# Performance work log

Measured on AMD Instinct MI355X. Metric: run time of the kernel, lower is better.

Reference implementation:

```python
import jax, jax.numpy as jnp
import numpy as np

L, H, D, V, TMAX = 12, 12, 768, 50257, 1024
B, T = 2, 1024
HD = D // H
EPS = 1e-5


def new_gelu(x):
    return 0.5 * x * (1.0 + jnp.tanh(jnp.sqrt(2.0 / jnp.pi) * (x + 0.044715 * x ** 3)))


def layer_norm(x, w, b):
    mu = jnp.mean(x, axis=-1, keepdims=True)
    var = jnp.var(x, axis=-1, keepdims=True)
    return (x - mu) * jax.lax.rsqrt(var + EPS) * w + b


def setup_inputs() -> dict:
    key = jax.random.key(0)
    ks = jax.random.split(key, 12)
    s = 0.02
    return {
        "idx": jax.random.randint(ks[0], (B, T), 0, V),
        "wte": jax.random.normal(ks[1], (V, D), jnp.float32) * s,
        "wpe": jax.random.normal(ks[2], (TMAX, D), jnp.float32) * s,
        "ln1_w": jnp.ones((L, D), jnp.float32),
        "ln1_b": jnp.zeros((L, D), jnp.float32),
        "attn_w": jax.random.normal(ks[3], (L, D, 3 * D), jnp.float32) * s,
        "attn_b": jnp.zeros((L, 3 * D), jnp.float32),
        "proj_w": jax.random.normal(ks[4], (L, D, D), jnp.float32) * (s / jnp.sqrt(2.0 * L)),
        "proj_b": jnp.zeros((L, D), jnp.float32),
        "ln2_w": jnp.ones((L, D), jnp.float32),
        "ln2_b": jnp.zeros((L, D), jnp.float32),
        "fc_w": jax.random.normal(ks[5], (L, D, 4 * D), jnp.float32) * s,
        "fc_b": jnp.zeros((L, 4 * D), jnp.float32),
        "fc2_w": jax.random.normal(ks[6], (L, 4 * D, D), jnp.float32) * (s / jnp.sqrt(2.0 * L)),
        "fc2_b": jnp.zeros((L, D), jnp.float32),
        "lnf_w": jnp.ones((D,), jnp.float32),
        "lnf_b": jnp.zeros((D,), jnp.float32),
        "lm_head_w": jax.random.normal(ks[7], (D, V), jnp.float32) * s,
    }


def _gpt_forward(idx, wte, wpe, ln1_w, ln1_b, attn_w, attn_b, proj_w, proj_b,
                 ln2_w, ln2_b, fc_w, fc_b, fc2_w, fc2_b, lnf_w, lnf_b, lm_head_w):
    b, t = idx.shape
    x = wte[idx] + wpe[:t][None, :, :]  # [B,T,D]
    causal = jnp.tril(jnp.ones((t, t), bool))  # [T,T]
    scale = 1.0 / jnp.sqrt(jnp.asarray(HD, x.dtype))

    layer_params = {
        "ln1_w": ln1_w, "ln1_b": ln1_b, "attn_w": attn_w, "attn_b": attn_b,
        "proj_w": proj_w, "proj_b": proj_b, "ln2_w": ln2_w, "ln2_b": ln2_b,
        "fc_w": fc_w, "fc_b": fc_b, "fc2_w": fc2_w, "fc2_b": fc2_b,
    }

    def block(x, p):
        h = layer_norm(x, p["ln1_w"], p["ln1_b"])
        qkv = h @ p["attn_w"] + p["attn_b"]  # [B,T,3D]
        q, k, v = jnp.split(qkv, 3, axis=-1)
        q = q.reshape(b, t, H, HD)
        k = k.reshape(b, t, H, HD)
        v = v.reshape(b, t, H, HD)
        att = jnp.einsum("bqhd,bkhd->bhqk", q, k) * scale
        att = jnp.where(causal[None, None, :, :], att, -jnp.inf)
        att = jax.nn.softmax(att, axis=-1)
        y = jnp.einsum("bhqk,bkhd->bqhd", att, v).reshape(b, t, D)
        x = x + y @ p["proj_w"] + p["proj_b"]
        h2 = layer_norm(x, p["ln2_w"], p["ln2_b"])
        m = new_gelu(h2 @ p["fc_w"] + p["fc_b"])
        x = x + m @ p["fc2_w"] + p["fc2_b"]
        return x, None

    x, _ = jax.lax.scan(block, x, layer_params)
    x = layer_norm(x, lnf_w, lnf_b)
    logits = x @ lm_head_w  # [B,T,V]
    return logits


def reference(idx, wte, wpe, ln1_w, ln1_b, attn_w, attn_b, proj_w, proj_b,
              ln2_w, ln2_b, fc_w, fc_b, fc2_w, fc2_b, lnf_w, lnf_b, lm_head_w):
    return _gpt_forward(idx, wte, wpe, ln1_w, ln1_b, attn_w, attn_b, proj_w, proj_b,
                        ln2_w, ln2_b, fc_w, fc_b, fc2_w, fc2_b, lnf_w, lnf_b, lm_head_w)
```

## Files before the change

kernel.cpp:

```cpp
#include <hip/hip_runtime.h>
#include <math.h>

#define Bsz  2
#define Tlen 1024
#define Dm   768
#define Hh   12
#define HDm  64
#define Ll   12
#define Vv   50257
#define Mrows (Bsz * Tlen)

typedef __attribute__((ext_vector_type(8))) short short8;
typedef __attribute__((ext_vector_type(4))) float f32x4;

__device__ __forceinline__ float bf2f(unsigned short u) {
  union { unsigned int i; float f; } v; v.i = ((unsigned int)u) << 16; return v.f;
}
__device__ __forceinline__ unsigned short f2bf(float f) {
  union { float f; unsigned int i; } v; v.f = f;
  unsigned int u = v.i;
  return (unsigned short)((u + 0x7FFFu + ((u >> 16) & 1u)) >> 16);
}
__device__ __forceinline__ float gelu_f(float x) {
  const float c = 0.7978845608028654f;
  return 0.5f * x * (1.0f + tanhf(c * (x + 0.044715f * x * x * x)));
}

__device__ __forceinline__ void gl_lds16(const unsigned short* g, unsigned short* l) {
  __builtin_amdgcn_global_load_lds(
      (const __attribute__((address_space(1))) unsigned int*)g,
      (__attribute__((address_space(3))) unsigned int*)l, 16, 0, 0);
}

__global__ void embed_kernel(const int* __restrict__ idx, const float* __restrict__ wte,
                             const float* __restrict__ wpe, float* __restrict__ x) {
  int i = (blockIdx.x * 256 + threadIdx.x) * 4;
  int d = i % Dm;
  int bt = i / Dm;
  int t = bt % Tlen;
  int tok = idx[bt];
  float4 a = *(const float4*)(wte + (size_t)tok * Dm + d);
  float4 p = *(const float4*)(wpe + (size_t)t * Dm + d);
  float4 r; r.x = a.x + p.x; r.y = a.y + p.y; r.z = a.z + p.z; r.w = a.w + p.w;
  *(float4*)(x + i) = r;
}

__global__ __launch_bounds__(256) void ln_wave(const float* __restrict__ x,
                                               const float* __restrict__ w,
                                               const float* __restrict__ b,
                                               unsigned short* __restrict__ out) {
  int tid = threadIdx.x, wv = tid >> 6, l = tid & 63;
  int row = blockIdx.x * 4 + wv;
  const float* xr = x + (size_t)row * Dm;
  float4 v[3];
  float s = 0.f, s2 = 0.f;
#pragma unroll
  for (int i = 0; i < 3; ++i) {
    v[i] = *(const float4*)(xr + l * 4 + i * 256);
    s += v[i].x + v[i].y + v[i].z + v[i].w;
    s2 += v[i].x * v[i].x + v[i].y * v[i].y + v[i].z * v[i].z + v[i].w * v[i].w;
  }
#pragma unroll
  for (int o = 1; o < 64; o <<= 1) {
    s += __shfl_xor(s, o, 64);
    s2 += __shfl_xor(s2, o, 64);
  }
  float mu = s * (1.0f / Dm);
  float var = s2 * (1.0f / Dm) - mu * mu;
  float rstd = rsqrtf(var + 1e-5f);
  unsigned short* yr = out + (size_t)row * Dm;
#pragma unroll
  for (int i = 0; i < 3; ++i) {
    float4 wv4 = *(const float4*)(w + l * 4 + i * 256);
    float4 bv4 = *(const float4*)(b + l * 4 + i * 256);
    ushort4 o4;
    o4.x = f2bf((v[i].x - mu) * rstd * wv4.x + bv4.x);
    o4.y = f2bf((v[i].y - mu) * rstd * wv4.y + bv4.y);
    o4.z = f2bf((v[i].z - mu) * rstd * wv4.z + bv4.z);
    o4.w = f2bf((v[i].w - mu) * rstd * wv4.w + bv4.w);
    *(ushort4*)(yr + l * 4 + i * 256) = o4;
  }
}

__global__ __launch_bounds__(256) void tconv_kernel(const float* __restrict__ W, int ldw,
                                                    int nValid, unsigned short* __restrict__ WT,
                                                    int K) {
  __shared__ float S[32][33];
  int n0 = blockIdx.x * 32, k0 = blockIdx.y * 32;
  int t = threadIdx.x;
  int nc = t & 31, kr0 = t >> 5;
#pragma unroll
  for (int i = 0; i < 4; ++i) {
    int kr = kr0 + i * 8;
    S[kr][nc] = (n0 + nc < nValid) ? W[(size_t)(k0 + kr) * ldw + n0 + nc] : 0.f;
  }
  __syncthreads();
  int r = t >> 3, c4 = (t & 7) * 4;
  ushort4 o;
  o.x = f2bf(S[c4 + 0][r]); o.y = f2bf(S[c4 + 1][r]);
  o.z = f2bf(S[c4 + 2][r]); o.w = f2bf(S[c4 + 3][r]);
  *(ushort4*)(WT + (size_t)(n0 + r) * K + k0 + c4) = o;
}

__global__ __launch_bounds__(256) void tconv4_kernel(
    const float* __restrict__ wA, const float* __restrict__ wP,
    const float* __restrict__ wF, const float* __restrict__ wF2,
    unsigned short* __restrict__ oA, unsigned short* __restrict__ oP,
    unsigned short* __restrict__ oF, unsigned short* __restrict__ oF2) {
  int bid = blockIdx.x;
  const float* W; unsigned short* WT; int ldw, K, ntn, local;
  if (bid < 1728)      { W = wA;  WT = oA;  ldw = 2304; K = 768;  ntn = 72; local = bid; }
  else if (bid < 2304) { W = wP;  WT = oP;  ldw = 768;  K = 768;  ntn = 24; local = bid - 1728; }
  else if (bid < 4608) { W = wF;  WT = oF;  ldw = 3072; K = 768;  ntn = 96; local = bid - 2304; }
  else                 { W = wF2; WT = oF2; ldw = 768;  K = 3072; ntn = 24; local = bid - 4608; }
  int n0 = (local % ntn) * 32, k0 = (local / ntn) * 32;
  __shared__ float S[32][33];
  int t = threadIdx.x;
  int nc = t & 31, kr0 = t >> 5;
#pragma unroll
  for (int i = 0; i < 4; ++i) {
    int kr = kr0 + i * 8;
    S[kr][nc] = W[(size_t)(k0 + kr) * ldw + n0 + nc];
  }
  __syncthreads();
  int r = t >> 3, c4 = (t & 7) * 4;
  ushort4 o;
  o.x = f2bf(S[c4 + 0][r]); o.y = f2bf(S[c4 + 1][r]);
  o.z = f2bf(S[c4 + 2][r]); o.w = f2bf(S[c4 + 3][r]);
  *(ushort4*)(WT + (size_t)(n0 + r) * K + k0 + c4) = o;
}

template<bool XMAP>
__global__ __launch_bounds__(256) void gemm_big(
    const unsigned short* __restrict__ A, const unsigned short* __restrict__ B, int K,
    const float* __restrict__ bias, const float* __restrict__ res,
    float* __restrict__ outF, unsigned short* __restrict__ outB,
    int ldc, int nValid, int act, int nColTiles) {
  int brow, bcol;
  if (XMAP) {
    int b = blockIdx.x, xcd = b & 7, slot = b >> 3;
    bcol = xcd + 8 * (slot >> 4);
    brow = slot & 15;
    if (bcol >= nColTiles) return;
  } else {
    bcol = blockIdx.x; brow = blockIdx.y;
  }
  __shared__ alignas(16) unsigned short As[2][128][32];
  __shared__ alignas(16) unsigned short Bs[2][128][32];
  int tid = threadIdx.x;
  int rowBase = brow * 128, colBase = bcol * 128;
  int w = tid >> 6, l = tid & 63;
  int wr = w >> 1, wc = w & 1;
  int srow = tid >> 2, skk = (tid & 3) * 8;
  const unsigned short* aSrc = A + (size_t)(rowBase + srow) * K + skk;
  const unsigned short* bSrc = B + (size_t)(colBase + srow) * K + skk;

  f32x4 acc[4][4];
#pragma unroll
  for (int m = 0; m < 4; ++m)
#pragma unroll
    for (int n = 0; n < 4; ++n) acc[m][n] = (f32x4){0.f, 0.f, 0.f, 0.f};

  int fr = l & 15, fq = l >> 4;

  gl_lds16(aSrc, &As[0][w * 16][0]);
  gl_lds16(aSrc + (size_t)64 * K, &As[0][w * 16 + 64][0]);
  gl_lds16(bSrc, &Bs[0][w * 16][0]);
  gl_lds16(bSrc + (size_t)64 * K, &Bs[0][w * 16 + 64][0]);

  int nIt = K >> 5;
  for (int it = 0; it < nIt; ++it) {
    int cur = it & 1;
    int k0 = it * 32;
    if (it + 1 < nIt) {
      int nx = cur ^ 1;
      gl_lds16(aSrc + k0 + 32, &As[nx][w * 16][0]);
      gl_lds16(aSrc + (size_t)64 * K + k0 + 32, &As[nx][w * 16 + 64][0]);
      gl_lds16(bSrc + k0 + 32, &Bs[nx][w * 16][0]);
      gl_lds16(bSrc + (size_t)64 * K + k0 + 32, &Bs[nx][w * 16 + 64][0]);
      asm volatile("s_waitcnt vmcnt(4)" ::: "memory");
    } else {
      asm volatile("s_waitcnt vmcnt(0)" ::: "memory");
    }
    asm volatile("s_barrier" ::: "memory");

    short8 af[4], bfr[4];
#pragma unroll
    for (int m = 0; m < 4; ++m)
      af[m] = *(const short8*)&As[cur][wr * 64 + m * 16 + fr][fq * 8];
#pragma unroll
    for (int n = 0; n < 4; ++n)
      bfr[n] = *(const short8*)&Bs[cur][wc * 64 + n * 16 + fr][fq * 8];
#pragma unroll
    for (int m = 0; m < 4; ++m)
#pragma unroll
      for (int n = 0; n < 4; ++n)
        acc[m][n] = __builtin_amdgcn_mfma_f32_16x16x32_bf16(af[m], bfr[n], acc[m][n], 0, 0, 0);
    asm volatile("s_barrier" ::: "memory");
  }

#pragma unroll
  for (int m = 0; m < 4; ++m) {
    int row = rowBase + wr * 64 + m * 16 + fq * 4;
#pragma unroll
    for (int n = 0; n < 4; ++n) {
      int col = colBase + wc * 64 + n * 16 + fr;
      if (col >= nValid) continue;
      float bv = bias ? bias[col] : 0.f;
#pragma unroll
      for (int j = 0; j < 4; ++j) {
        float v = acc[m][n][j] + bv;
        if (act) v = gelu_f(v);
        if (res) v += res[(size_t)(row + j) * ldc + col];
        if (outF) outF[(size_t)(row + j) * ldc + col] = v;
        else      outB[(size_t)(row + j) * ldc + col] = f2bf(v);
      }
    }
  }
}

__global__ __launch_bounds__(256) void gemm_bf16_sm(
    const unsigned short* __restrict__ A, const unsigned short* __restrict__ B, int K,
    const float* __restrict__ bias, const float* __restrict__ res,
    float* __restrict__ outF, unsigned short* __restrict__ outB,
    int ldc, int act) {
  __shared__ alignas(16) unsigned short As[2][64][32];
  __shared__ alignas(16) unsigned short Bs[2][128][32];
  int tid = threadIdx.x;
  int rowBase = blockIdx.y * 64;
  int colBase = blockIdx.x * 128;
  int w = tid >> 6, l = tid & 63;
  int fr = l & 15, fq = l >> 4;

  int srow = l >> 2, skk = (l & 3) * 8;
  const unsigned short* aSrc = A + (size_t)(rowBase + w * 16 + srow) * K + skk;
  const unsigned short* bSrc = B + (size_t)(colBase + w * 16 + srow) * K + skk;

  f32x4 acc[4][2];
#pragma unroll
  for (int m = 0; m < 4; ++m)
#pragma unroll
    for (int n = 0; n < 2; ++n) acc[m][n] = (f32x4){0.f, 0.f, 0.f, 0.f};

  gl_lds16(aSrc, &As[0][w * 16][0]);
  gl_lds16(bSrc, &Bs[0][w * 16][0]);
  gl_lds16(bSrc + (size_t)64 * K, &Bs[0][w * 16 + 64][0]);

  int nIt = K >> 5;
  for (int it = 0; it < nIt; ++it) {
    int cur = it & 1;
    int k0 = it * 32;
    if (it + 1 < nIt) {
      int nx = cur ^ 1;
      gl_lds16(aSrc + k0 + 32, &As[nx][w * 16][0]);
      gl_lds16(bSrc + k0 + 32, &Bs[nx][w * 16][0]);
      gl_lds16(bSrc + (size_t)64 * K + k0 + 32, &Bs[nx][w * 16 + 64][0]);
      asm volatile("s_waitcnt vmcnt(3)" ::: "memory");
    } else {
      asm volatile("s_waitcnt vmcnt(0)" ::: "memory");
    }
    asm volatile("s_barrier" ::: "memory");

    short8 af[4], bfr[2];
#pragma unroll
    for (int m = 0; m < 4; ++m)
      af[m] = *(const short8*)&As[cur][m * 16 + fr][fq * 8];
#pragma unroll
    for (int n = 0; n < 2; ++n)
      bfr[n] = *(const short8*)&Bs[cur][w * 32 + n * 16 + fr][fq * 8];
#pragma unroll
    for (int m = 0; m < 4; ++m)
#pragma unroll
      for (int n = 0; n < 2; ++n)
        acc[m][n] = __builtin_amdgcn_mfma_f32_16x16x32_bf16(af[m], bfr[n], acc[m][n], 0, 0, 0);
    asm volatile("s_barrier" ::: "memory");
  }

#pragma unroll
  for (int m = 0; m < 4; ++m) {
    int row = rowBase + m * 16 + fq * 4;
#pragma unroll
    for (int n = 0; n < 2; ++n) {
      int col = colBase + w * 32 + n * 16 + fr;
      float bv = bias ? bias[col] : 0.f;
#pragma unroll
      for (int j = 0; j < 4; ++j) {
        float v = acc[m][n][j] + bv;
        if (act) v = gelu_f(v);
        if (res) v += res[(size_t)(row + j) * ldc + col];
        if (outF) outF[(size_t)(row + j) * ldc + col] = v;
        else      outB[(size_t)(row + j) * ldc + col] = f2bf(v);
      }
    }
  }
}

__global__ __launch_bounds__(256) void attn_mfma(const unsigned short* __restrict__ qkv,
                                                 unsigned short* __restrict__ y) {
  int bx = blockIdx.x;
  int qt = bx & 15;
  int h  = (bx >> 4) % Hh;
  int b  = bx / (16 * Hh);
  int q0 = qt * 64;
  int tid = threadIdx.x;
  int w = tid >> 6, l = tid & 63;
  int g = l >> 4, fr = l & 15;

  __shared__ alignas(16) unsigned short Kl[2][4096];
  __shared__ alignas(16) unsigned short Vt[4096];
  __shared__ alignas(16) unsigned short Pl[4][1024];

  const size_t rs = 3 * Dm;
  const unsigned short* base = qkv + (size_t)(b * Tlen) * rs + h * HDm;

  short8 qf[2];
  {
    const unsigned short* qrow = base + (size_t)(q0 + w * 16 + fr) * rs;
    qf[0] = *(const short8*)(qrow + g * 8);
    qf[1] = *(const short8*)(qrow + g * 8 + 32);
  }

  int vt_t = tid >> 2, vt_dc = tid & 3;
  uint4 v0r, v1r;

  f32x4 oAcc[4];
#pragma unroll
  for (int nd = 0; nd < 4; ++nd) oAcc[nd] = (f32x4){0.f, 0.f, 0.f, 0.f};
  float mRun[4] = {-1e30f, -1e30f, -1e30f, -1e30f};
  float lRun[4] = {0.f, 0.f, 0.f, 0.f};

  unsigned short* Pw = &Pl[w][0];
  int nkt = qt + 1;

  {
#pragma unroll
    for (int i = 0; i < 2; ++i) {
      int c = i * 256 + tid;
      int t = c >> 3, cl = c & 7;
      int dch = cl ^ (t & 7);
      gl_lds16(base + (size_t)t * rs + Dm + dch * 8, &Kl[0][(i * 256 + w * 64) * 8]);
    }
    const unsigned short* p = base + (size_t)vt_t * rs + 2 * Dm + vt_dc * 16;
    v0r = *(const uint4*)p;
    v1r = *(const uint4*)(p + 8);
  }

  for (int kt = 0; kt < nkt; ++kt) {
    int cur = kt & 1;
    int kbase = kt * 64;
    asm volatile("s_waitcnt vmcnt(0)" ::: "memory");
    __builtin_amdgcn_s_barrier();

    {
      union { uint4 u; unsigned short s[8]; } a, bb;
      a.u = v0r; bb.u = v1r;
#pragma unroll
      for (int j = 0; j < 8; ++j) {
        int d = vt_dc * 16 + j;
        Vt[d * 64 + (vt_t ^ ((d & 7) << 3))] = a.s[j];
        int d2 = d + 8;
        Vt[d2 * 64 + (vt_t ^ ((d2 & 7) << 3))] = bb.s[j];
      }
    }
    if (kt + 1 < nkt) {
      int kb = kbase + 64;
#pragma unroll
      for (int i = 0; i < 2; ++i) {
        int c = i * 256 + tid;
        int t = c >> 3, cl = c & 7;
        int dch = cl ^ (t & 7);
        gl_lds16(base + (size_t)(kb + t) * rs + Dm + dch * 8,
                 &Kl[cur ^ 1][(i * 256 + w * 64) * 8]);
      }
      const unsigned short* p = base + (size_t)(kb + vt_t) * rs + 2 * Dm + vt_dc * 16;
      v0r = *(const uint4*)p;
      v1r = *(const uint4*)(p + 8);
    }
    asm volatile("s_waitcnt lgkmcnt(0)" ::: "memory");
    __builtin_amdgcn_s_barrier();

    f32x4 sAcc[4];
#pragma unroll
    for (int nt = 0; nt < 4; ++nt) sAcc[nt] = (f32x4){0.f, 0.f, 0.f, 0.f};
#pragma unroll
    for (int ks = 0; ks < 2; ++ks)
#pragma unroll
      for (int nt = 0; nt < 4; ++nt) {
        int kcol = nt * 16 + fr;
        short8 kf = *(const short8*)&Kl[cur][kcol * 64 + ((g * 8 + ks * 32) ^ ((kcol & 7) << 3))];
        sAcc[nt] = __builtin_amdgcn_mfma_f32_16x16x32_bf16(qf[ks], kf, sAcc[nt], 0, 0, 0);
      }

    float corr[4];
#pragma unroll
    for (int j = 0; j < 4; ++j) {
      int qg = q0 + w * 16 + g * 4 + j;
      float tm = -1e30f;
#pragma unroll
      for (int nt = 0; nt < 4; ++nt) {
        float s = sAcc[nt][j] * 0.125f;
        int tg = kbase + nt * 16 + fr;
        if (tg > qg) s = -1e30f;
        sAcc[nt][j] = s;
        tm = fmaxf(tm, s);
      }
      tm = fmaxf(tm, __shfl_xor(tm, 1, 16));
      tm = fmaxf(tm, __shfl_xor(tm, 2, 16));
      tm = fmaxf(tm, __shfl_xor(tm, 4, 16));
      tm = fmaxf(tm, __shfl_xor(tm, 8, 16));
      float mN = fmaxf(mRun[j], tm);
      corr[j] = __expf(mRun[j] - mN);
      mRun[j] = mN;
      float ps = 0.f;
#pragma unroll
      for (int nt = 0; nt < 4; ++nt) {
        float p = __expf(sAcc[nt][j] - mN);
        sAcc[nt][j] = p;
        ps += p;
      }
      ps += __shfl_xor(ps, 1, 16);
      ps += __shfl_xor(ps, 2, 16);
      ps += __shfl_xor(ps, 4, 16);
      ps += __shfl_xor(ps, 8, 16);
      lRun[j] = lRun[j] * corr[j] + ps;
    }

#pragma unroll
    for (int nt = 0; nt < 4; ++nt)
#pragma unroll
      for (int j = 0; j < 4; ++j) {
        int q = g * 4 + j;
        int t = nt * 16 + fr;
        Pw[q * 64 + (t ^ ((q & 7) << 3))] = f2bf(sAcc[nt][j]);
      }
#pragma unroll
    for (int nd = 0; nd < 4; ++nd)
#pragma unroll
      for (int j = 0; j < 4; ++j) oAcc[nd][j] *= corr[j];

#pragma unroll
    for (int ks = 0; ks < 2; ++ks) {
      short8 pf = *(const short8*)&Pw[fr * 64 + ((g * 8 + ks * 32) ^ ((fr & 7) << 3))];
#pragma unroll
      for (int nd = 0; nd < 4; ++nd) {
        int d = nd * 16 + fr;
        short8 vf = *(const short8*)&Vt[d * 64 + ((g * 8 + ks * 32) ^ ((fr & 7) << 3))];
        oAcc[nd] = __builtin_amdgcn_mfma_f32_16x16x32_bf16(pf, vf, oAcc[nd], 0, 0, 0);
      }
    }
  }

#pragma unroll
  for (int j = 0; j < 4; ++j) {
    float inv = 1.0f / lRun[j];
    int q = q0 + w * 16 + g * 4 + j;
    unsigned short* yr = y + (size_t)(b * Tlen + q) * Dm + h * HDm + fr;
#pragma unroll
    for (int nd = 0; nd < 4; ++nd)
      yr[nd * 16] = f2bf(oAcc[nd][j] * inv);
  }
}

extern "C" void kernel_launch(void* const* d_in, const int* in_sizes, int n_in,
                              void* d_out, int out_size, void* d_ws, size_t ws_size,
                              hipStream_t stream) {
  const int*   idx    = (const int*)d_in[0];
  const float* wte    = (const float*)d_in[1];
  const float* wpe    = (const float*)d_in[2];
  const float* ln1_w  = (const float*)d_in[3];
  const float* ln1_b  = (const float*)d_in[4];
  const float* attn_w = (const float*)d_in[5];
  const float* attn_b = (const float*)d_in[6];
  const float* proj_w = (const float*)d_in[7];
  const float* proj_b = (const float*)d_in[8];
  const float* ln2_w  = (const float*)d_in[9];
  const float* ln2_b  = (const float*)d_in[10];
  const float* fc_w   = (const float*)d_in[11];
  const float* fc_b   = (const float*)d_in[12];
  const float* fc2_w  = (const float*)d_in[13];
  const float* fc2_b  = (const float*)d_in[14];
  const float* lnf_w  = (const float*)d_in[15];
  const float* lnf_b  = (const float*)d_in[16];
  const float* lmw    = (const float*)d_in[17];
  float* out = (float*)d_out;

  float* x = (float*)d_ws;
  unsigned short* qkvb = (unsigned short*)(x + (size_t)Mrows * Dm);
  unsigned short* xb   = qkvb + (size_t)Mrows * 3 * Dm;
  unsigned short* yb   = xb + (size_t)Mrows * Dm;
  unsigned short* mb   = yb + (size_t)Mrows * Dm;
  unsigned short* wbuf = mb + (size_t)Mrows * 4 * Dm;
  unsigned short* wAttn = wbuf;
  unsigned short* wProj = wAttn + (size_t)3 * Dm * Dm;
  unsigned short* wFc   = wProj + (size_t)Dm * Dm;
  unsigned short* wFc2  = wFc + (size_t)4 * Dm * Dm;

  const size_t baseBytes = (size_t)Mrows * Dm * 4 + (size_t)Mrows * 9 * Dm * 2;
  size_t availShorts = (ws_size - baseBytes) / 2;
  long long cc = (long long)(availShorts / Dm) & ~127LL;
  if (cc > 50304) cc = 50304;
  const int chunkCols = (int)cc;

  embed_kernel<<<(Mrows * Dm) / 1024, 256, 0, stream>>>(idx, wte, wpe, x);

  for (int l = 0; l < Ll; ++l) {
    tconv4_kernel<<<6912, 256, 0, stream>>>(
        attn_w + (size_t)l * Dm * 3 * Dm, proj_w + (size_t)l * Dm * Dm,
        fc_w + (size_t)l * Dm * 4 * Dm, fc2_w + (size_t)l * 4 * Dm * Dm,
        wAttn, wProj, wFc, wFc2);

    ln_wave<<<Mrows / 4, 256, 0, stream>>>(x, ln1_w + l * Dm, ln1_b + l * Dm, xb);
    gemm_bf16_sm<<<dim3(18, 32), 256, 0, stream>>>(xb, wAttn, Dm, attn_b + (size_t)l * 3 * Dm,
                                                   nullptr, nullptr, qkvb, 3 * Dm, 0);
    attn_mfma<<<Bsz * Hh * 16, 256, 0, stream>>>(qkvb, yb);
    gemm_bf16_sm<<<dim3(6, 32), 256, 0, stream>>>(yb, wProj, Dm, proj_b + (size_t)l * Dm,
                                                  x, x, nullptr, Dm, 0);
    ln_wave<<<Mrows / 4, 256, 0, stream>>>(x, ln2_w + l * Dm, ln2_b + l * Dm, xb);
    gemm_bf16_sm<<<dim3(24, 32), 256, 0, stream>>>(xb, wFc, Dm, fc_b + (size_t)l * 4 * Dm,
                                                   nullptr, nullptr, mb, 4 * Dm, 1);
    gemm_bf16_sm<<<dim3(6, 32), 256, 0, stream>>>(mb, wFc2, 4 * Dm, fc2_b + (size_t)l * Dm,
                                                  x, x, nullptr, Dm, 0);
  }

  ln_wave<<<Mrows / 4, 256, 0, stream>>>(x, lnf_w, lnf_b, xb);
  for (int base = 0; base < Vv; base += chunkCols) {
    int ncv = Vv - base; if (ncv > chunkCols) ncv = chunkCols;
    int ntiles = (ncv + 127) / 128;
    tconv_kernel<<<dim3((ncv + 31) / 32, 24), 256, 0, stream>>>(lmw + base, Vv, ncv, wbuf, Dm);
    int cpx = (ntiles + 7) / 8;
    gemm_big<true><<<8 * 16 * cpx, 256, 0, stream>>>(
        xb, wbuf, Dm, nullptr, nullptr, out + base, nullptr, Vv, ncv, 0, ntiles);
  }
}
```

Before: 2.595 ms.

## Swizzle GEMM LDS layout, add split-K atomic residual GEMMs, reorder attention blocks

Applies an XOR swizzle to the K-slot of the LDS tiles in both GEMM kernels to cut LDS bank conflicts on the MFMA fragment reads. Adds a split-K GEMM that accumulates the proj and fc2 outputs into the residual stream with float atomics, doubling the block count for these low-occupancy N=768 GEMMs. Reorders attention block scheduling so the longest causal query tiles start first. Atomic accumulation makes the float summation order nondeterministic and adds atomic traffic.

```diff
diff --git a/kernel.cpp b/kernel.cpp
--- a/kernel.cpp
+++ b/kernel.cpp
@@ -31,6 +31,7 @@
       (const __attribute__((address_space(1))) unsigned int*)g,
       (__attribute__((address_space(3))) unsigned int*)l, 16, 0, 0);
 }
+
 
 __global__ void embed_kernel(const int* __restrict__ idx, const float* __restrict__ wte,
                              const float* __restrict__ wpe, float* __restrict__ x) {
@@ -151,7 +152,8 @@
   int rowBase = brow * 128, colBase = bcol * 128;
   int w = tid >> 6, l = tid & 63;
   int wr = w >> 1, wc = w & 1;
-  int srow = tid >> 2, skk = (tid & 3) * 8;
+  int srow = tid >> 2;
+  int skk = (((tid & 3) ^ ((tid >> 3) & 3))) * 8;
   const unsigned short* aSrc = A + (size_t)(rowBase + srow) * K + skk;
   const unsigned short* bSrc = B + (size_t)(colBase + srow) * K + skk;
 
@@ -162,6 +164,7 @@
     for (int n = 0; n < 4; ++n) acc[m][n] = (f32x4){0.f, 0.f, 0.f, 0.f};
 
   int fr = l & 15, fq = l >> 4;
+  int kslot = (fq ^ ((fr >> 1) & 3)) * 8;
 
   gl_lds16(aSrc, &As[0][w * 16][0]);
   gl_lds16(aSrc + (size_t)64 * K, &As[0][w * 16 + 64][0]);
@@ -187,10 +190,10 @@
     short8 af[4], bfr[4];
 #pragma unroll
     for (int m = 0; m < 4; ++m)
-      af[m] = *(const short8*)&As[cur][wr * 64 + m * 16 + fr][fq * 8];
+      af[m] = *(const short8*)&As[cur][wr * 64 + m * 16 + fr][kslot];
 #pragma unroll
     for (int n = 0; n < 4; ++n)
-      bfr[n] = *(const short8*)&Bs[cur][wc * 64 + n * 16 + fr][fq * 8];
+      bfr[n] = *(const short8*)&Bs[cur][wc * 64 + n * 16 + fr][kslot];
 #pragma unroll
     for (int m = 0; m < 4; ++m)
 #pragma unroll
@@ -221,7 +224,7 @@
 
 __global__ __launch_bounds__(256) void gemm_bf16_sm(
     const unsigned short* __restrict__ A, const unsigned short* __restrict__ B, int K,
-    const float* __restrict__ bias, const float* __restrict__ res,
+    const float* __restrict__ bias,
     float* __restrict__ outF, unsigned short* __restrict__ outB,
     int ldc, int act) {
   __shared__ alignas(16) unsigned short As[2][64][32];
@@ -232,9 +235,11 @@
   int w = tid >> 6, l = tid & 63;
   int fr = l & 15, fq = l >> 4;
 
-  int srow = l >> 2, skk = (l & 3) * 8;
+  int srow = l >> 2;
+  int skk = (((l & 3) ^ ((l >> 3) & 3))) * 8;
   const unsigned short* aSrc = A + (size_t)(rowBase + w * 16 + srow) * K + skk;
   const unsigned short* bSrc = B + (size_t)(colBase + w * 16 + srow) * K + skk;
+  int kslot = (fq ^ ((fr >> 1) & 3)) * 8;
 
   f32x4 acc[4][2];
 #pragma unroll
@@ -264,10 +269,10 @@
     short8 af[4], bfr[2];
 #pragma unroll
     for (int m = 0; m < 4; ++m)
-      af[m] = *(const short8*)&As[cur][m * 16 + fr][fq * 8];
+      af[m] = *(const short8*)&As[cur][m * 16 + fr][kslot];
 #pragma unroll
     for (int n = 0; n < 2; ++n)
-      bfr[n] = *(const short8*)&Bs[cur][w * 32 + n * 16 + fr][fq * 8];
+      bfr[n] = *(const short8*)&Bs[cur][w * 32 + n * 16 + fr][kslot];
 #pragma unroll
     for (int m = 0; m < 4; ++m)
 #pragma unroll
@@ -287,9 +292,82 @@
       for (int j = 0; j < 4; ++j) {
         float v = acc[m][n][j] + bv;
         if (act) v = gelu_f(v);
-        if (res) v += res[(size_t)(row + j) * ldc + col];
         if (outF) outF[(size_t)(row + j) * ldc + col] = v;
         else      outB[(size_t)(row + j) * ldc + col] = f2bf(v);
+      }
+    }
+  }
+}
+
+__global__ __launch_bounds__(256) void gemm_splitk(
+    const unsigned short* __restrict__ A, const unsigned short* __restrict__ B, int K,
+    int Klen, const float* __restrict__ bias, float* __restrict__ outF, int ldc) {
+  __shared__ alignas(16) unsigned short As[2][64][32];
+  __shared__ alignas(16) unsigned short Bs[2][128][32];
+  int tid = threadIdx.x;
+  int rowBase = blockIdx.y * 64;
+  int colBase = blockIdx.x * 128;
+  int Koff = blockIdx.z * Klen;
+  int w = tid >> 6, l = tid & 63;
+  int fr = l & 15, fq = l >> 4;
+
+  int srow = l >> 2;
+  int skk = (((l & 3) ^ ((l >> 3) & 3))) * 8;
+  const unsigned short* aSrc = A + (size_t)(rowBase + w * 16 + srow) * K + Koff + skk;
+  const unsigned short* bSrc = B + (size_t)(colBase + w * 16 + srow) * K + Koff + skk;
+  int kslot = (fq ^ ((fr >> 1) & 3)) * 8;
+
+  f32x4 acc[4][2];
+#pragma unroll
+  for (int m = 0; m < 4; ++m)
+#pragma unroll
+    for (int n = 0; n < 2; ++n) acc[m][n] = (f32x4){0.f, 0.f, 0.f, 0.f};
+
+  gl_lds16(aSrc, &As[0][w * 16][0]);
+  gl_lds16(bSrc, &Bs[0][w * 16][0]);
+  gl_lds16(bSrc + (size_t)64 * K, &Bs[0][w * 16 + 64][0]);
+
+  int nIt = Klen >> 5;
+  for (int it = 0; it < nIt; ++it) {
+    int cur = it & 1;
+    int k0 = it * 32;
+    if (it + 1 < nIt) {
+      int nx = cur ^ 1;
+      gl_lds16(aSrc + k0 + 32, &As[nx][w * 16][0]);
+      gl_lds16(bSrc + k0 + 32, &Bs[nx][w * 16][0]);
+      gl_lds16(bSrc + (size_t)64 * K + k0 + 32, &Bs[nx][w * 16 + 64][0]);
+      asm volatile("s_waitcnt vmcnt(3)" ::: "memory");
+    } else {
+      asm volatile("s_waitcnt vmcnt(0)" ::: "memory");
+    }
+    asm volatile("s_barrier" ::: "memory");
+
+    short8 af[4], bfr[2];
+#pragma unroll
+    for (int m = 0; m < 4; ++m)
+      af[m] = *(const short8*)&As[cur][m * 16 + fr][kslot];
+#pragma unroll
+    for (int n = 0; n < 2; ++n)
+      bfr[n] = *(const short8*)&Bs[cur][w * 32 + n * 16 + fr][kslot];
+#pragma unroll
+    for (int m = 0; m < 4; ++m)
+#pragma unroll
+      for (int n = 0; n < 2; ++n)
+        acc[m][n] = __builtin_amdgcn_mfma_f32_16x16x32_bf16(af[m], bfr[n], acc[m][n], 0, 0, 0);
+    asm volatile("s_barrier" ::: "memory");
+  }
+
+  bool addBias = (blockIdx.z == 0);
+#pragma unroll
+  for (int m = 0; m < 4; ++m) {
+    int row = rowBase + m * 16 + fq * 4;
+#pragma unroll
+    for (int n = 0; n < 2; ++n) {
+      int col = colBase + w * 32 + n * 16 + fr;
+      float bv = addBias ? bias[col] : 0.f;
+#pragma unroll
+      for (int j = 0; j < 4; ++j) {
+        unsafeAtomicAdd(&outF[(size_t)(row + j) * ldc + col], acc[m][n][j] + bv);
       }
     }
   }
@@ -298,9 +376,10 @@
 __global__ __launch_bounds__(256) void attn_mfma(const unsigned short* __restrict__ qkv,
                                                  unsigned short* __restrict__ y) {
   int bx = blockIdx.x;
-  int qt = bx & 15;
-  int h  = (bx >> 4) % Hh;
-  int b  = bx / (16 * Hh);
+  int qt = 15 - (bx / 24);
+  int bh = bx % 24;
+  int h  = bh % Hh;
+  int b  = bh / Hh;
   int q0 = qt * 64;
   int tid = threadIdx.x;
   int w = tid >> 6, l = tid & 63;
@@ -511,15 +590,15 @@
 
     ln_wave<<<Mrows / 4, 256, 0, stream>>>(x, ln1_w + l * Dm, ln1_b + l * Dm, xb);
     gemm_bf16_sm<<<dim3(18, 32), 256, 0, stream>>>(xb, wAttn, Dm, attn_b + (size_t)l * 3 * Dm,
-                                                   nullptr, nullptr, qkvb, 3 * Dm, 0);
+                                                   nullptr, qkvb, 3 * Dm, 0);
     attn_mfma<<<Bsz * Hh * 16, 256, 0, stream>>>(qkvb, yb);
-    gemm_bf16_sm<<<dim3(6, 32), 256, 0, stream>>>(yb, wProj, Dm, proj_b + (size_t)l * Dm,
-                                                  x, x, nullptr, Dm, 0);
+    gemm_splitk<<<dim3(6, 32, 2), 256, 0, stream>>>(yb, wProj, Dm, Dm / 2,
+                                                    proj_b + (size_t)l * Dm, x, Dm);
     ln_wave<<<Mrows / 4, 256, 0, stream>>>(x, ln2_w + l * Dm, ln2_b + l * Dm, xb);
     gemm_bf16_sm<<<dim3(24, 32), 256, 0, stream>>>(xb, wFc, Dm, fc_b + (size_t)l * 4 * Dm,
-                                                   nullptr, nullptr, mb, 4 * Dm, 1);
-    gemm_bf16_sm<<<dim3(6, 32), 256, 0, stream>>>(mb, wFc2, 4 * Dm, fc2_b + (size_t)l * Dm,
-                                                  x, x, nullptr, Dm, 0);
+                                                   nullptr, mb, 4 * Dm, 1);
+    gemm_splitk<<<dim3(6, 32, 2), 256, 0, stream>>>(mb, wFc2, 4 * Dm, 2 * Dm,
+                                                    fc2_b + (size_t)l * Dm, x, Dm);
   }
 
   ln_wave<<<Mrows / 4, 256, 0, stream>>>(x, lnf_w, lnf_b, xb);
```

Result: faster. 2.166 ms (-16.5%).
